# Optimization experiments

Hardware: AMD Instinct MI355X
Metric: run time of the kernel (lower is better)

## Reference

```python
import jax, jax.numpy as jnp
import numpy as np
import itertools as it

K = 10          # delay taps
SKIP = 2        # stride between taps
TRANSIENTS = 100
P = 3           # monomial degree

# monomial index table: all degree-P combinations_with_replacement of the K linear features
_MONOM_IDX = jnp.asarray(list(it.combinations_with_replacement(range(K), P)), dtype=jnp.int32)  # [nlin_dim, P]


def setup_inputs() -> dict:
    key = jax.random.key(0)
    X = jax.random.normal(key, (8, 4, 4096), dtype=jnp.float32)  # [batch, row, n_steps]
    return {"X": X}


def reference(X):
    # X: [b, r, n]; n_dim = 1 after the original unsqueeze(3)
    b, r, n = X.shape
    pad = (K - 1) * SKIP
    # zero-padded delay embedding replaces the roll loop:
    # lin_features[b,r,i,j] = X[b,r, i - (K-1-j)*SKIP], zero for negative time
    Xpad = jnp.pad(X, ((0, 0), (0, 0), (pad, 0)))           # [b, r, n+pad]
    idx = jnp.arange(n)[:, None] + jnp.arange(K)[None, :] * SKIP  # [n, K]
    lin_features = Xpad[:, :, idx]                          # [b, r, n, K]
    # monomial (degree-P) features: gather then product over the small P axis
    nlin_features = jnp.prod(lin_features[..., _MONOM_IDX], axis=-1)  # [b, r, n, nlin_dim]
    tot = jnp.concatenate([lin_features, nlin_features], axis=3)[:, :, TRANSIENTS:, :]
    ones = jnp.ones(tot.shape[:3] + (1,), dtype=tot.dtype)  # bias column
    return jnp.concatenate([ones, tot], axis=3)             # [b, r, n-TRANSIENTS, 1+K+nlin_dim]
```

## Files before the change

kernel.cpp:

```cpp
#include <hip/hip_runtime.h>

#define KTAPS 10
#define SKIP  2
#define TRANS 100
#define PAD   ((KTAPS - 1) * SKIP)
#define NFEAT 231
#define NIN   4096
#define NT    (NIN - TRANS)
#define NROWS 32
#define TT    32

template<int PLO, int PHI, bool LIN>
__device__ __forceinline__ void emit_features(const float* __restrict__ tap,
                                              float* __restrict__ frow) {
    if (LIN) {
        frow[0] = 1.0f;
#pragma unroll
        for (int k = 0; k < KTAPS; ++k) frow[1 + k] = tap[k];
    }
    int p = 0, fb = 1 + KTAPS;
#pragma unroll
    for (int i = 0; i < KTAPS; ++i) {
#pragma unroll
        for (int j = i; j < KTAPS; ++j) {
            if (p >= PLO && p < PHI) {
                const float pij = tap[i] * tap[j];
#pragma unroll
                for (int l = j; l < KTAPS; ++l)
                    frow[fb + (l - j)] = pij * tap[l];
            }
            fb += KTAPS - j;
            ++p;
        }
    }
}

__global__ __launch_bounds__(256, 5) void nvar_kernel(const float* __restrict__ X,
                                                      float* __restrict__ out) {
    __shared__ float feat[TT * NFEAT];

    const int tile = blockIdx.x;
    const int row  = blockIdx.y;
    const int t0   = tile * TT;
    const int tcount = min(TT, NT - t0);

    const int tl = threadIdx.x & 31;
    const int wq = threadIdx.x >> 6;

    int tg = t0 + tl;
    if (tg >= NT) tg = NT - 1;

    const float* xrow = X + (size_t)row * NIN;
    float tap[KTAPS];
#pragma unroll
    for (int k = 0; k < KTAPS; ++k)
        tap[k] = xrow[tg + (TRANS - PAD) + 2 * k];

    float* frow = feat + tl * NFEAT;
    switch (wq) {
        case 0:  emit_features< 0,  6, true >(tap, frow); break;
        case 1:  emit_features< 6, 19, false>(tap, frow); break;
        case 2:  emit_features<19, 31, false>(tap, frow); break;
        default: emit_features<31, 55, false>(tap, frow); break;
    }

    __syncthreads();

    const int total4 = (tcount * NFEAT) >> 2;
    float4* __restrict__ o4 =
        reinterpret_cast<float4*>(out + ((size_t)row * NT + t0) * NFEAT);
    const float4* s4 = reinterpret_cast<const float4*>(feat);
    for (int i = threadIdx.x; i < total4; i += 256)
        o4[i] = s4[i];
}

extern "C" void kernel_launch(void* const* d_in, const int* in_sizes, int n_in,
                              void* d_out, int out_size, void* d_ws, size_t ws_size,
                              hipStream_t stream) {
    const float* X = (const float*)d_in[0];
    float* out = (float*)d_out;
    dim3 grid((NT + TT - 1) / TT, NROWS);
    nvar_kernel<<<grid, 256, 0, stream>>>(X, out);
}
```

Measured before the change: 121.3 us.

## Use single-wave blocks with one thread computing all features per timestep

Replaces the 256-thread block, where four wave groups each computed a slice of the monomials for 32 timesteps, with a 64-thread block. There each of 40 active lanes computes all 231 features for its own timestep, the tile grows from 32 to 40 timesteps, and the copy loop is unrolled. The aim is to drop the redundant tap loads and the switch divergence across waves and to raise the number of blocks resident per CU. In exchange 24 of the 64 lanes sit idle during compute, each thread makes more serial stores to LDS, and each block has fewer threads to drive the global stores.

Result: slower. 125.1 us (+3.1%).

```diff
diff --git a/kernel.cpp b/kernel.cpp
--- a/kernel.cpp
+++ b/kernel.cpp
@@ -8,60 +8,48 @@
 #define NIN   4096
 #define NT    (NIN - TRANS)
 #define NROWS 32
-#define TT    32
+#define TT    40
+#define NTILES ((NT + TT - 1) / TT)
 
-template<int PLO, int PHI, bool LIN>
-__device__ __forceinline__ void emit_features(const float* __restrict__ tap,
-                                              float* __restrict__ frow) {
-    if (LIN) {
-        frow[0] = 1.0f;
-#pragma unroll
-        for (int k = 0; k < KTAPS; ++k) frow[1 + k] = tap[k];
-    }
-    int p = 0, fb = 1 + KTAPS;
-#pragma unroll
-    for (int i = 0; i < KTAPS; ++i) {
-#pragma unroll
-        for (int j = i; j < KTAPS; ++j) {
-            if (p >= PLO && p < PHI) {
-                const float pij = tap[i] * tap[j];
-#pragma unroll
-                for (int l = j; l < KTAPS; ++l)
-                    frow[fb + (l - j)] = pij * tap[l];
-            }
-            fb += KTAPS - j;
-            ++p;
-        }
-    }
-}
-
-__global__ __launch_bounds__(256, 5) void nvar_kernel(const float* __restrict__ X,
-                                                      float* __restrict__ out) {
-    __shared__ float feat[TT * NFEAT];
+__global__ __launch_bounds__(64) void nvar_kernel(const float* __restrict__ X,
+                                                  float* __restrict__ out) {
+    __shared__ __align__(16) float feat[TT * NFEAT];
 
     const int tile = blockIdx.x;
     const int row  = blockIdx.y;
     const int t0   = tile * TT;
     const int tcount = min(TT, NT - t0);
 
-    const int tl = threadIdx.x & 31;
-    const int wq = threadIdx.x >> 6;
+    const int tl = threadIdx.x;
+    const float* xrow = X + (size_t)row * NIN;
 
-    int tg = t0 + tl;
-    if (tg >= NT) tg = NT - 1;
+    if (tl < TT) {
+        int tg = t0 + tl;
+        if (tg >= NT) tg = NT - 1;
 
-    const float* xrow = X + (size_t)row * NIN;
-    float tap[KTAPS];
+        float tap[KTAPS];
 #pragma unroll
-    for (int k = 0; k < KTAPS; ++k)
-        tap[k] = xrow[tg + (TRANS - PAD) + 2 * k];
+        for (int k = 0; k < KTAPS; ++k)
+            tap[k] = xrow[tg + (TRANS - PAD) + 2 * k];
 
-    float* frow = feat + tl * NFEAT;
-    switch (wq) {
-        case 0:  emit_features< 0,  6, true >(tap, frow); break;
-        case 1:  emit_features< 6, 19, false>(tap, frow); break;
-        case 2:  emit_features<19, 31, false>(tap, frow); break;
-        default: emit_features<31, 55, false>(tap, frow); break;
+        float* frow = feat + tl * NFEAT;
+        frow[0] = 1.0f;
+#pragma unroll
+        for (int k = 0; k < KTAPS; ++k)
+            frow[1 + k] = tap[k];
+
+        int fb = 1 + KTAPS;
+#pragma unroll
+        for (int i = 0; i < KTAPS; ++i) {
+#pragma unroll
+            for (int j = i; j < KTAPS; ++j) {
+                const float pij = tap[i] * tap[j];
+#pragma unroll
+                for (int l = j; l < KTAPS; ++l)
+                    frow[fb + (l - j)] = pij * tap[l];
+                fb += KTAPS - j;
+            }
+        }
     }
 
     __syncthreads();
@@ -70,7 +58,8 @@
     float4* __restrict__ o4 =
         reinterpret_cast<float4*>(out + ((size_t)row * NT + t0) * NFEAT);
     const float4* s4 = reinterpret_cast<const float4*>(feat);
-    for (int i = threadIdx.x; i < total4; i += 256)
+#pragma unroll 4
+    for (int i = threadIdx.x; i < total4; i += 64)
         o4[i] = s4[i];
 }
 
@@ -79,6 +68,6 @@
                               hipStream_t stream) {
     const float* X = (const float*)d_in[0];
     float* out = (float*)d_out;
-    dim3 grid((NT + TT - 1) / TT, NROWS);
-    nvar_kernel<<<grid, 256, 0, stream>>>(X, out);
+    dim3 grid(NTILES, NROWS);
+    nvar_kernel<<<grid, 64, 0, stream>>>(X, out);
 }
```
